# Kernel optimization log

Hardware: AMD Instinct MI355X
Metric: run time of the kernel (lower is better)

The kernel has to match this reference:

```python
import jax, jax.numpy as jnp
import numpy as np

# MoE config (matches init_kwargs)
T = 16384   # tokens
H = 1024    # hidden size
I = 1024    # intermediate size per expert
E = 8       # n_experts
TOPK = 2
RENORMALIZE = True


def setup_inputs() -> dict:
    key = jax.random.key(0)
    ks = jax.random.split(key, 6)
    x = jax.random.normal(ks[0], (T, H), dtype=jnp.float32)
    gating_output = jax.random.normal(ks[1], (T, E), dtype=jnp.float32)
    # fp8-quantized weights simulated as their integer-grid values in fp32;
    # dequant = q * per-expert scalar scale (normalize_e4m3fn_to_native_float8 path)
    w1 = jax.random.normal(ks[2], (E, 2 * I, H), dtype=jnp.float32)  # fused [gate; up]
    w2 = jax.random.normal(ks[3], (E, H, I), dtype=jnp.float32)      # down_proj
    w1_scale = jax.random.uniform(ks[4], (E,), dtype=jnp.float32, minval=0.01, maxval=0.05)
    w2_scale = jax.random.uniform(ks[5], (E,), dtype=jnp.float32, minval=0.01, maxval=0.05)
    return {"x": x, "gating_output": gating_output, "w1": w1, "w2": w2,
            "w1_scale": w1_scale, "w2_scale": w2_scale}


def _moe(x, gating_output, w1, w2, w1_scale, w2_scale):
    # softmax scoring -> top-k routing (use_grouped_topk=False)
    probs = jax.nn.softmax(gating_output, axis=-1)              # [T, E]
    topk_w, topk_idx = jax.lax.top_k(probs, TOPK)               # [T, K]
    if RENORMALIZE:
        topk_w = topk_w / jnp.sum(topk_w, axis=-1, keepdims=True)
    out = jnp.zeros_like(x)
    for e in range(E):  # fixed small expert count: grouped-GEMM reference
        w1e = w1[e] * w1_scale[e]                               # dequant [2I, H]
        w2e = w2[e] * w2_scale[e]                               # dequant [H, I]
        gate = x @ w1e[:I].T                                    # [T, I]
        up = x @ w1e[I:].T                                      # [T, I]
        h = jax.nn.silu(gate) * up                              # SwiGLU
        y = h @ w2e.T                                           # [T, H]
        # per-token routing weight for this expert (0 if not routed)
        coef = jnp.sum(jnp.where(topk_idx == e, topk_w, 0.0), axis=-1)  # [T]
        out = out + coef[:, None] * y
    return out


def reference(x, gating_output, w1, w2, w1_scale, w2_scale):
    return _moe(x, gating_output, w1, w2, w1_scale, w2_scale)
```

## Files before the change

### kernel.cpp

```cpp
#include <hip/hip_runtime.h>
#include <hip/hip_bf16.h>

#define T_TOK 16384
#define H_DIM 1024
#define I_DIM 1024
#define E_NUM 8
#define NPAIR (T_TOK * 2)
#define BM 128
#define BK 64
#define MAX_MT (NPAIR / BM + E_NUM)

typedef float v4f __attribute__((ext_vector_type(4)));
typedef float v16f __attribute__((ext_vector_type(16)));
typedef short v8s __attribute__((ext_vector_type(8)));

__device__ __forceinline__ unsigned short f2bf(float f) {
    unsigned int u = __float_as_uint(f);
    unsigned int r = (u + 0x7fffu + ((u >> 16) & 1u)) >> 16;
    return (unsigned short)r;
}
__device__ __forceinline__ float bf2f(unsigned short s) {
    return __uint_as_float(((unsigned int)s) << 16);
}

__device__ __forceinline__ void gl_lds16(const void* g, void* l) {
    __builtin_amdgcn_global_load_lds(
        (const __attribute__((address_space(1))) void*)g,
        (__attribute__((address_space(3))) void*)l, 16, 0, 0);
}

__device__ __forceinline__ int swz(int row, int unit) {
    return row * 64 + ((unit ^ (row & 7)) << 3);
}

__global__ void k_route(const float* __restrict__ gating,
                        int* __restrict__ tokExp, float* __restrict__ tokW,
                        int* __restrict__ counts) {
    int t = blockIdx.x * 256 + threadIdx.x;
    int lane = threadIdx.x & 63;
    float g[E_NUM];
#pragma unroll
    for (int e = 0; e < E_NUM; e++) g[e] = gating[t * E_NUM + e];
    int i0 = 0; float v0 = g[0];
#pragma unroll
    for (int e = 1; e < E_NUM; e++) if (g[e] > v0) { v0 = g[e]; i0 = e; }
    int i1 = -1; float v1 = -1e30f;
#pragma unroll
    for (int e = 0; e < E_NUM; e++) if (e != i0 && g[e] > v1) { v1 = g[e]; i1 = e; }
    float w0 = 1.f / (1.f + __expf(v1 - v0));
    tokExp[2 * t] = i0; tokExp[2 * t + 1] = i1;
    tokW[2 * t] = w0;   tokW[2 * t + 1] = 1.f - w0;
#pragma unroll
    for (int e = 0; e < E_NUM; e++) {
        unsigned long long mA = __ballot(i0 == e);
        unsigned long long mB = __ballot(i1 == e);
        int c = __popcll(mA) + __popcll(mB);
        if (lane == 0 && c) atomicAdd(&counts[e], c);
    }
}

__global__ void k_scan(const int* __restrict__ counts, int* __restrict__ offsets,
                       int* __restrict__ tileOff, int* __restrict__ cursor) {
    if (threadIdx.x == 0 && blockIdx.x == 0) {
        int o = 0, to = 0;
        for (int e = 0; e < E_NUM; e++) {
            offsets[e] = o; tileOff[e] = to; cursor[e] = o;
            o += counts[e];
            to += (counts[e] + BM - 1) / BM;
        }
        offsets[E_NUM] = o; tileOff[E_NUM] = to;
    }
}

__global__ void k_scatter(const int* __restrict__ tokExp, const float* __restrict__ tokW,
                          int* __restrict__ cursor,
                          int* __restrict__ pairTok, float* __restrict__ pairW,
                          int* __restrict__ invMap) {
    int t = blockIdx.x * 256 + threadIdx.x;
    int lane = threadIdx.x & 63;
#pragma unroll
    for (int k = 0; k < 2; k++) {
        int e = tokExp[2 * t + k];
        int pos = 0;
#pragma unroll
        for (int ex = 0; ex < E_NUM; ex++) {
            unsigned long long m = __ballot(e == ex);
            if (m) {
                int leader = __builtin_ctzll(m);
                int base = 0;
                if (lane == leader) base = atomicAdd(&cursor[ex], __popcll(m));
                base = __shfl(base, leader);
                if (e == ex) pos = base + __popcll(m & ((1ull << lane) - 1ull));
            }
        }
        pairTok[pos] = t;
        pairW[pos] = tokW[2 * t + k];
        invMap[2 * t + k] = pos;
    }
}

__global__ void k_cvt_x(const float* __restrict__ src, unsigned short* __restrict__ dst) {
    size_t i4 = ((size_t)blockIdx.x * 256 + threadIdx.x) * 4;
    float4 v = *(const float4*)(src + i4);
    ushort4 o;
    o.x = f2bf(v.x); o.y = f2bf(v.y); o.z = f2bf(v.z); o.w = f2bf(v.w);
    *(ushort4*)(dst + i4) = o;
}

__global__ void k_cvt_w(const float* __restrict__ src, unsigned short* __restrict__ dst,
                        const float* __restrict__ scale, int shift) {
    size_t i4 = ((size_t)blockIdx.x * 256 + threadIdx.x) * 4;
    float s = scale[i4 >> shift];
    float4 v = *(const float4*)(src + i4);
    ushort4 o;
    o.x = f2bf(v.x * s); o.y = f2bf(v.y * s); o.z = f2bf(v.z * s); o.w = f2bf(v.w * s);
    *(ushort4*)(dst + i4) = o;
}

__global__ __launch_bounds__(512, 4)
void k_gemm1(const unsigned short* __restrict__ xbf,
             const unsigned short* __restrict__ w1bf,
             const int* __restrict__ pairTok,
             const int* __restrict__ offsets, const int* __restrict__ tileOff,
             unsigned short* __restrict__ hbuf) {
    __shared__ unsigned short lA[BM * BK];
    __shared__ unsigned short lB[256 * BK];

    int mt = blockIdx.x;
    if (mt >= tileOff[E_NUM]) return;
    int e = 0;
    while (mt >= tileOff[e + 1]) e++;
    int row0 = offsets[e] + (mt - tileOff[e]) * BM;
    int valid = offsets[e + 1] - row0; if (valid > BM) valid = BM;

    int nt = blockIdx.y;
    int tid = threadIdx.x;
    int lane = tid & 63, wave = tid >> 6;
    int role = wave >> 2, quad = wave & 3;
    int wm = quad >> 1, wn = quad & 1;

    int lr = lane >> 3;
    int lcs = ((lane & 7) ^ lr) * 8;

    const unsigned short* wg = w1bf + (size_t)e * 2 * I_DIM * H_DIM + (size_t)(nt * 128) * H_DIM;
    const unsigned short* wu = wg + (size_t)I_DIM * H_DIM;

    int tokRow[2];
#pragma unroll
    for (int j = 0; j < 2; j++) {
        int r = wave * 16 + j * 8 + lr;
        int rc = r < valid ? r : valid - 1;
        tokRow[j] = pairTok[row0 + rc];
    }
    const unsigned short* bRow[4];
#pragma unroll
    for (int j = 0; j < 4; j++) {
        int brow = wave * 32 + j * 8 + lr;
        bRow[j] = (brow < 128) ? (wg + (size_t)brow * H_DIM)
                               : (wu + (size_t)(brow - 128) * H_DIM);
    }

    v16f acc[2][2];
#pragma unroll
    for (int i = 0; i < 2; i++)
#pragma unroll
        for (int j = 0; j < 2; j++) acc[i][j] = (v16f)0.f;

    for (int ko = 0; ko < H_DIM / BK; ko++) {
        int k0 = ko * BK;
        __syncthreads();
#pragma unroll
        for (int j = 0; j < 2; j++)
            gl_lds16(xbf + (size_t)tokRow[j] * H_DIM + k0 + lcs, lA + (wave * 2 + j) * 512);
#pragma unroll
        for (int j = 0; j < 4; j++)
            gl_lds16(bRow[j] + k0 + lcs, lB + (wave * 4 + j) * 512);
        __syncthreads();
#pragma unroll
        for (int kk = 0; kk < BK; kk += 16) {
            int u = (kk >> 3) + (lane >> 5);
            v8s a[2], b[2];
#pragma unroll
            for (int i = 0; i < 2; i++)
                a[i] = *(const v8s*)(lA + swz(wm * 64 + i * 32 + (lane & 31), u));
#pragma unroll
            for (int j = 0; j < 2; j++)
                b[j] = *(const v8s*)(lB + swz(role * 128 + wn * 64 + j * 32 + (lane & 31), u));
#pragma unroll
            for (int i = 0; i < 2; i++)
#pragma unroll
                for (int j = 0; j < 2; j++)
                    acc[i][j] = __builtin_amdgcn_mfma_f32_32x32x16_bf16(a[i], b[j], acc[i][j], 0, 0, 0);
        }
    }

    int half = lane >> 5, c = lane & 31;
    __syncthreads();
    if (role == 1) {
#pragma unroll
        for (int i = 0; i < 2; i++)
#pragma unroll
            for (int r = 0; r < 16; r++) {
                int row = wm * 64 + i * 32 + (r & 3) + 8 * (r >> 2) + 4 * half;
#pragma unroll
                for (int j = 0; j < 2; j++)
                    lB[row * 128 + wn * 64 + j * 32 + c] = f2bf(acc[i][j][r]);
            }
    }
    __syncthreads();
    if (role == 0) {
#pragma unroll
        for (int i = 0; i < 2; i++)
#pragma unroll
            for (int r = 0; r < 16; r++) {
                int row = wm * 64 + i * 32 + (r & 3) + 8 * (r >> 2) + 4 * half;
                if (row < valid) {
                    size_t base = (size_t)(row0 + row) * I_DIM + nt * 128;
#pragma unroll
                    for (int j = 0; j < 2; j++) {
                        float g = acc[i][j][r];
                        float uu = bf2f(lB[row * 128 + wn * 64 + j * 32 + c]);
                        float s = g / (1.f + __expf(-g));
                        hbuf[base + wn * 64 + j * 32 + c] = f2bf(s * uu);
                    }
                }
            }
    }
}

__global__ __launch_bounds__(512, 4)
void k_gemm2(const unsigned short* __restrict__ hbuf,
             const unsigned short* __restrict__ w2bf,
             const float* __restrict__ pairW,
             const int* __restrict__ offsets, const int* __restrict__ tileOff,
             unsigned short* __restrict__ ybuf) {
    __shared__ unsigned short lA[BM * BK];
    __shared__ unsigned short lB[256 * BK];

    int mt = blockIdx.x;
    if (mt >= tileOff[E_NUM]) return;
    int e = 0;
    while (mt >= tileOff[e + 1]) e++;
    int row0 = offsets[e] + (mt - tileOff[e]) * BM;
    int valid = offsets[e + 1] - row0; if (valid > BM) valid = BM;

    int nt = blockIdx.y;
    int tid = threadIdx.x;
    int lane = tid & 63, wave = tid >> 6;
    int wm = wave >> 2, wn = wave & 3;

    int lr = lane >> 3;
    int lcs = ((lane & 7) ^ lr) * 8;

    const unsigned short* w2e = w2bf + (size_t)e * H_DIM * I_DIM + (size_t)(nt * 256) * I_DIM;

    int rowA[2];
#pragma unroll
    for (int j = 0; j < 2; j++) {
        int r = wave * 16 + j * 8 + lr;
        int rc = r < valid ? r : valid - 1;
        rowA[j] = row0 + rc;
    }

    v16f acc[2][2];
#pragma unroll
    for (int i = 0; i < 2; i++)
#pragma unroll
        for (int j = 0; j < 2; j++) acc[i][j] = (v16f)0.f;

    for (int ko = 0; ko < I_DIM / BK; ko++) {
        int k0 = ko * BK;
        __syncthreads();
#pragma unroll
        for (int j = 0; j < 2; j++)
            gl_lds16(hbuf + (size_t)rowA[j] * I_DIM + k0 + lcs, lA + (wave * 2 + j) * 512);
#pragma unroll
        for (int j = 0; j < 4; j++)
            gl_lds16(w2e + (size_t)(wave * 32 + j * 8 + lr) * I_DIM + k0 + lcs,
                     lB + (wave * 4 + j) * 512);
        __syncthreads();
#pragma unroll
        for (int kk = 0; kk < BK; kk += 16) {
            int u = (kk >> 3) + (lane >> 5);
            v8s a[2], b[2];
#pragma unroll
            for (int i = 0; i < 2; i++)
                a[i] = *(const v8s*)(lA + swz(wm * 64 + i * 32 + (lane & 31), u));
#pragma unroll
            for (int j = 0; j < 2; j++)
                b[j] = *(const v8s*)(lB + swz(wn * 64 + j * 32 + (lane & 31), u));
#pragma unroll
            for (int i = 0; i < 2; i++)
#pragma unroll
                for (int j = 0; j < 2; j++)
                    acc[i][j] = __builtin_amdgcn_mfma_f32_32x32x16_bf16(a[i], b[j], acc[i][j], 0, 0, 0);
        }
    }

    int half = lane >> 5, c = lane & 31;
#pragma unroll
    for (int i = 0; i < 2; i++)
#pragma unroll
        for (int r = 0; r < 16; r++) {
            int row = wm * 64 + i * 32 + (r & 3) + 8 * (r >> 2) + 4 * half;
            if (row < valid) {
                int pos = row0 + row;
                float coef = pairW[pos];
                unsigned short* orow = ybuf + (size_t)pos * H_DIM + nt * 256;
#pragma unroll
                for (int j = 0; j < 2; j++)
                    orow[wn * 64 + j * 32 + c] = f2bf(coef * acc[i][j][r]);
            }
        }
}

__global__ __launch_bounds__(256)
void k_reduce(const unsigned short* __restrict__ ybuf,
              const int* __restrict__ invMap,
              float* __restrict__ out) {
    int t = blockIdx.x;
    int p0 = invMap[2 * t], p1 = invMap[2 * t + 1];
    int c4 = threadIdx.x * 4;
    ushort4 a = *(const ushort4*)(ybuf + (size_t)p0 * H_DIM + c4);
    ushort4 b = *(const ushort4*)(ybuf + (size_t)p1 * H_DIM + c4);
    float4 o;
    o.x = bf2f(a.x) + bf2f(b.x);
    o.y = bf2f(a.y) + bf2f(b.y);
    o.z = bf2f(a.z) + bf2f(b.z);
    o.w = bf2f(a.w) + bf2f(b.w);
    *(float4*)(out + (size_t)t * H_DIM + c4) = o;
}

extern "C" void kernel_launch(void* const* d_in, const int* in_sizes, int n_in,
                              void* d_out, int out_size, void* d_ws, size_t ws_size,
                              hipStream_t stream) {
    const float* x      = (const float*)d_in[0];
    const float* gating = (const float*)d_in[1];
    const float* w1     = (const float*)d_in[2];
    const float* w2     = (const float*)d_in[3];
    const float* w1s    = (const float*)d_in[4];
    const float* w2s    = (const float*)d_in[5];
    float* out = (float*)d_out;

    char* ws = (char*)d_ws;
    size_t off = 0;
    auto alloc = [&](size_t bytes) { void* p = ws + off; off += (bytes + 255) & ~(size_t)255; return p; };
    unsigned short* xbf  = (unsigned short*)alloc((size_t)T_TOK * H_DIM * 2);
    unsigned short* w1bf = (unsigned short*)alloc((size_t)E_NUM * 2 * I_DIM * H_DIM * 2);
    unsigned short* w2bf = (unsigned short*)alloc((size_t)E_NUM * H_DIM * I_DIM * 2);
    unsigned short* hbuf = (unsigned short*)alloc((size_t)NPAIR * I_DIM * 2);
    unsigned short* ybuf = (unsigned short*)alloc((size_t)NPAIR * H_DIM * 2);
    int*   pairTok  = (int*)alloc(NPAIR * 4);
    float* pairW    = (float*)alloc(NPAIR * 4);
    int*   tokExp   = (int*)alloc(NPAIR * 4);
    float* tokW     = (float*)alloc(NPAIR * 4);
    int*   invMap   = (int*)alloc(NPAIR * 4);
    int*   counts   = (int*)alloc(64);
    int*   offsets  = (int*)alloc(64);
    int*   tileOff  = (int*)alloc(64);
    int*   cursor   = (int*)alloc(64);

    hipMemsetAsync(counts, 0, 64, stream);

    k_route<<<T_TOK / 256, 256, 0, stream>>>(gating, tokExp, tokW, counts);
    k_scan<<<1, 64, 0, stream>>>(counts, offsets, tileOff, cursor);
    k_scatter<<<T_TOK / 256, 256, 0, stream>>>(tokExp, tokW, cursor, pairTok, pairW, invMap);
    k_cvt_x<<<(T_TOK * H_DIM / 4) / 256, 256, 0, stream>>>(x, xbf);
    k_cvt_w<<<(E_NUM * 2 * I_DIM * H_DIM / 4) / 256, 256, 0, stream>>>(w1, w1bf, w1s, 21);
    k_cvt_w<<<(E_NUM * H_DIM * I_DIM / 4) / 256, 256, 0, stream>>>(w2, w2bf, w2s, 20);

    dim3 g1(MAX_MT, I_DIM / 128);
    k_gemm1<<<g1, 512, 0, stream>>>(xbf, w1bf, pairTok, offsets, tileOff, hbuf);
    dim3 g2(MAX_MT, H_DIM / 256);
    k_gemm2<<<g2, 512, 0, stream>>>(hbuf, w2bf, pairW, offsets, tileOff, ybuf);
    k_reduce<<<T_TOK, 256, 0, stream>>>(ybuf, invMap, out);
}
```

Measured before the change: 561.1 us.

## Fuse conversion kernels, swizzle LDS epilogue, split gemm1 launch in halves

Merges the three fp32-to-bf16 conversion kernels into one launch that handles eight elements per thread. It also XOR-swizzles the LDS staging of the up-projection accumulator in gemm1's epilogue to cut bank conflicts. Finally, gemm1 is split into two launches over halves of the M-tile range via a new tile-base argument. The split adds launch overhead and a possible tail, and the fused conversion adds a per-thread branch.

After: 581.8 us. +3.7%, slower.

```diff
diff --git a/kernel.cpp b/kernel.cpp
--- a/kernel.cpp
+++ b/kernel.cpp
@@ -13,6 +13,7 @@
 typedef float v4f __attribute__((ext_vector_type(4)));
 typedef float v16f __attribute__((ext_vector_type(16)));
 typedef short v8s __attribute__((ext_vector_type(8)));
+typedef unsigned short u8s __attribute__((ext_vector_type(8)));
 
 __device__ __forceinline__ unsigned short f2bf(float f) {
     unsigned int u = __float_as_uint(f);
@@ -99,22 +100,25 @@
     }
 }
 
-__global__ void k_cvt_x(const float* __restrict__ src, unsigned short* __restrict__ dst) {
-    size_t i4 = ((size_t)blockIdx.x * 256 + threadIdx.x) * 4;
-    float4 v = *(const float4*)(src + i4);
-    ushort4 o;
-    o.x = f2bf(v.x); o.y = f2bf(v.y); o.z = f2bf(v.z); o.w = f2bf(v.w);
-    *(ushort4*)(dst + i4) = o;
-}
-
-__global__ void k_cvt_w(const float* __restrict__ src, unsigned short* __restrict__ dst,
-                        const float* __restrict__ scale, int shift) {
-    size_t i4 = ((size_t)blockIdx.x * 256 + threadIdx.x) * 4;
-    float s = scale[i4 >> shift];
-    float4 v = *(const float4*)(src + i4);
-    ushort4 o;
-    o.x = f2bf(v.x * s); o.y = f2bf(v.y * s); o.z = f2bf(v.z * s); o.w = f2bf(v.w * s);
-    *(ushort4*)(dst + i4) = o;
+__global__ void k_cvt_all(const float* __restrict__ x,
+                          const float* __restrict__ w1, const float* __restrict__ w2,
+                          const float* __restrict__ w1s, const float* __restrict__ w2s,
+                          unsigned short* __restrict__ xbf,
+                          unsigned short* __restrict__ w1bf,
+                          unsigned short* __restrict__ w2bf) {
+    const size_t N0 = (size_t)T_TOK * H_DIM;
+    const size_t N1 = (size_t)E_NUM * 2 * I_DIM * H_DIM;
+    size_t i8 = ((size_t)blockIdx.x * 256 + threadIdx.x) * 8;
+    const float* src; unsigned short* dst; size_t off; float s;
+    if (i8 < N0)            { src = x;  dst = xbf;  off = i8;           s = 1.f; }
+    else if (i8 < N0 + N1)  { src = w1; dst = w1bf; off = i8 - N0;      s = w1s[off >> 21]; }
+    else                    { src = w2; dst = w2bf; off = i8 - N0 - N1; s = w2s[off >> 20]; }
+    float4 v0 = *(const float4*)(src + off);
+    float4 v1 = *(const float4*)(src + off + 4);
+    u8s o;
+    o[0] = f2bf(v0.x * s); o[1] = f2bf(v0.y * s); o[2] = f2bf(v0.z * s); o[3] = f2bf(v0.w * s);
+    o[4] = f2bf(v1.x * s); o[5] = f2bf(v1.y * s); o[6] = f2bf(v1.z * s); o[7] = f2bf(v1.w * s);
+    *(u8s*)(dst + off) = o;
 }
 
 __global__ __launch_bounds__(512, 4)
@@ -122,11 +126,12 @@
              const unsigned short* __restrict__ w1bf,
              const int* __restrict__ pairTok,
              const int* __restrict__ offsets, const int* __restrict__ tileOff,
-             unsigned short* __restrict__ hbuf) {
+             unsigned short* __restrict__ hbuf,
+             int mtBase) {
     __shared__ unsigned short lA[BM * BK];
     __shared__ unsigned short lB[256 * BK];
 
-    int mt = blockIdx.x;
+    int mt = blockIdx.x + mtBase;
     if (mt >= tileOff[E_NUM]) return;
     int e = 0;
     while (mt >= tileOff[e + 1]) e++;
@@ -203,8 +208,10 @@
             for (int r = 0; r < 16; r++) {
                 int row = wm * 64 + i * 32 + (r & 3) + 8 * (r >> 2) + 4 * half;
 #pragma unroll
-                for (int j = 0; j < 2; j++)
-                    lB[row * 128 + wn * 64 + j * 32 + c] = f2bf(acc[i][j][r]);
+                for (int j = 0; j < 2; j++) {
+                    int cs = (j * 32 + c) ^ ((row & 4) << 3);
+                    lB[row * 128 + wn * 64 + cs] = f2bf(acc[i][j][r]);
+                }
             }
     }
     __syncthreads();
@@ -219,7 +226,8 @@
 #pragma unroll
                     for (int j = 0; j < 2; j++) {
                         float g = acc[i][j][r];
-                        float uu = bf2f(lB[row * 128 + wn * 64 + j * 32 + c]);
+                        int cs = (j * 32 + c) ^ ((row & 4) << 3);
+                        float uu = bf2f(lB[row * 128 + wn * 64 + cs]);
                         float s = g / (1.f + __expf(-g));
                         hbuf[base + wn * 64 + j * 32 + c] = f2bf(s * uu);
                     }
@@ -365,12 +373,16 @@
     k_route<<<T_TOK / 256, 256, 0, stream>>>(gating, tokExp, tokW, counts);
     k_scan<<<1, 64, 0, stream>>>(counts, offsets, tileOff, cursor);
     k_scatter<<<T_TOK / 256, 256, 0, stream>>>(tokExp, tokW, cursor, pairTok, pairW, invMap);
-    k_cvt_x<<<(T_TOK * H_DIM / 4) / 256, 256, 0, stream>>>(x, xbf);
-    k_cvt_w<<<(E_NUM * 2 * I_DIM * H_DIM / 4) / 256, 256, 0, stream>>>(w1, w1bf, w1s, 21);
-    k_cvt_w<<<(E_NUM * H_DIM * I_DIM / 4) / 256, 256, 0, stream>>>(w2, w2bf, w2s, 20);
-
-    dim3 g1(MAX_MT, I_DIM / 128);
-    k_gemm1<<<g1, 512, 0, stream>>>(xbf, w1bf, pairTok, offsets, tileOff, hbuf);
+
+    size_t ncvt = ((size_t)T_TOK * H_DIM + (size_t)E_NUM * 2 * I_DIM * H_DIM +
+                   (size_t)E_NUM * H_DIM * I_DIM) / 8 / 256;
+    k_cvt_all<<<(int)ncvt, 256, 0, stream>>>(x, w1, w2, w1s, w2s, xbf, w1bf, w2bf);
+
+    int halfMT = MAX_MT / 2;
+    dim3 g1(halfMT, I_DIM / 128);
+    k_gemm1<<<g1, 512, 0, stream>>>(xbf, w1bf, pairTok, offsets, tileOff, hbuf, 0);
+    k_gemm1<<<g1, 512, 0, stream>>>(xbf, w1bf, pairTok, offsets, tileOff, hbuf, halfMT);
+
     dim3 g2(MAX_MT, H_DIM / 256);
     k_gemm2<<<g2, 512, 0, stream>>>(hbuf, w2bf, pairW, offsets, tileOff, ybuf);
     k_reduce<<<T_TOK, 256, 0, stream>>>(ybuf, invMap, out);
```
